# Performance work log

Hardware: AMD Instinct MI355X
Metric: run time of the kernel (lower is better)

The kernel has to match this reference:

```python
import jax, jax.numpy as jnp
import numpy as np

C = 256
NH = 4  # attention heads
G = 8   # groupnorm groups
EPS = 1e-5


def group_norm(x, weight, bias):
    B, Cc, H, W = x.shape
    xg = x.reshape(B, G, Cc // G, H, W)
    mean = xg.mean(axis=(2, 3, 4), keepdims=True)
    var = xg.var(axis=(2, 3, 4), keepdims=True)
    xg = (xg - mean) * jax.lax.rsqrt(var + EPS)
    xn = xg.reshape(B, Cc, H, W)
    return xn * weight[None, :, None, None] + bias[None, :, None, None]


def setup_inputs() -> dict:
    key = jax.random.key(0)
    ks = jax.random.split(key, 7)
    B, H, W = 16, 32, 32
    x = jax.random.normal(ks[0], (B, C, H, W), dtype=jnp.float32)
    n_weight = jnp.ones((C,), dtype=jnp.float32)
    n_bias = jnp.zeros((C,), dtype=jnp.float32)
    qkv_w = jax.random.normal(ks[1], (3 * C, C), dtype=jnp.float32) * (C ** -0.5)
    qkv_b = jnp.zeros((3 * C,), dtype=jnp.float32)
    p_w = jax.random.normal(ks[2], (C, C), dtype=jnp.float32) * (C ** -0.5)
    p_b = jnp.zeros((C,), dtype=jnp.float32)
    return {"x": x, "n_weight": n_weight, "n_bias": n_bias,
            "qkv_w": qkv_w, "qkv_b": qkv_b, "p_w": p_w, "p_b": p_b}


def reference(x, n_weight, n_bias, qkv_w, qkv_b, p_w, p_b):
    B, Cc, H, W = x.shape
    N = H * W
    dh = Cc // NH
    sc = dh ** -0.5
    xn = group_norm(x, n_weight, n_bias)  # [B,C,H,W]
    xn_flat = xn.reshape(B, Cc, N)
    # 1x1 conv == channel matmul
    qkv = jnp.einsum('oc,bcn->bon', qkv_w, xn_flat) + qkv_b[None, :, None]
    qkv = qkv.reshape(B, 3, NH, dh, N)
    q, k, v = qkv[:, 0], qkv[:, 1], qkv[:, 2]  # [B,h,dh,N]
    a = jax.nn.softmax(jnp.einsum('bhci,bhcj->bhij', q, k) * sc, axis=-1)
    o = jnp.einsum('bhij,bhcj->bhci', a, v).reshape(B, Cc, N)
    proj = jnp.einsum('oc,bcn->bon', p_w, o) + p_b[None, :, None]
    return x + proj.reshape(B, Cc, H, W)
```

## Files before the change

kernel.cpp:

```cpp
#include <hip/hip_runtime.h>
#include <math.h>

typedef unsigned short ushort;
typedef unsigned int uint;
typedef __attribute__((ext_vector_type(8))) short bf16x8;
typedef __attribute__((ext_vector_type(4))) float f32x4;

constexpr int Bc  = 16;
constexpr float EPSc = 1e-5f;

__device__ inline ushort f2bf(float f) {
    uint u = __float_as_uint(f);
    uint r = (u + 0x7fffu + ((u >> 16) & 1u)) >> 16;
    return (ushort)r;
}
__device__ inline uint pack2(float a, float b) {
    return (uint)f2bf(a) | ((uint)f2bf(b) << 16);
}
__device__ __forceinline__ void gl_lds16(const ushort* g, ushort* l) {
    __builtin_amdgcn_global_load_lds(
        (const __attribute__((address_space(1))) void*)g,
        (__attribute__((address_space(3))) void*)l, 16, 0, 0);
}

__global__ __launch_bounds__(256) void pre_k(
    const float* __restrict__ x, const float* __restrict__ qkvw,
    const float* __restrict__ pw, float* __restrict__ pstats,
    ushort* __restrict__ wqb, ushort* __restrict__ pwb) {
    int blk = blockIdx.x;
    if (blk < 512) {
        int bg = blk >> 2, part = blk & 3;
        const float4* p = (const float4*)(x + (size_t)bg * 32768 + part * 8192);
        float s = 0.f, s2 = 0.f;
        for (int i = threadIdx.x; i < 2048; i += 256) {
            float4 v = p[i];
            s += v.x + v.y + v.z + v.w;
            s2 += v.x*v.x + v.y*v.y + v.z*v.z + v.w*v.w;
        }
        __shared__ float rs[256], rq[256];
        rs[threadIdx.x] = s; rq[threadIdx.x] = s2;
        __syncthreads();
        for (int off = 128; off > 0; off >>= 1) {
            if (threadIdx.x < (unsigned)off) {
                rs[threadIdx.x] += rs[threadIdx.x + off];
                rq[threadIdx.x] += rq[threadIdx.x + off];
            }
            __syncthreads();
        }
        if (threadIdx.x == 0) {
            pstats[blk * 2]     = rs[0];
            pstats[blk * 2 + 1] = rq[0];
        }
    } else {
        int idx = ((blk - 512) * 256 + threadIdx.x) * 4;
        if (idx < 196608) {
            int row = idx >> 8;
            float sc = (row < 256) ? 0.125f : 1.f;
            float4 v = *(const float4*)&qkvw[idx];
            uint2 u; u.x = pack2(v.x * sc, v.y * sc); u.y = pack2(v.z * sc, v.w * sc);
            *(uint2*)&wqb[idx] = u;
        } else {
            int j = idx - 196608;
            float4 v = *(const float4*)&pw[j];
            uint2 u; u.x = pack2(v.x, v.y); u.y = pack2(v.z, v.w);
            *(uint2*)&pwb[j] = u;
        }
    }
}

__global__ __launch_bounds__(256) void norm_t_k(
    const float* __restrict__ x, const float* __restrict__ pstats,
    const float* __restrict__ nw, const float* __restrict__ nb,
    ushort* __restrict__ xt) {
    int b = blockIdx.z, ct = blockIdx.y, nt = blockIdx.x;
    __shared__ ushort T[64 * 72];
    int t = threadIdx.x;
    int nn4 = (t & 15) * 4;
#pragma unroll
    for (int p = 0; p < 4; ++p) {
        int cl = (t >> 4) + p * 16;
        int c = ct * 64 + cl;
        int g = c >> 5;
        int base = (b * 8 + g) * 8;
        float s  = (pstats[base] + pstats[base+2]) + (pstats[base+4] + pstats[base+6]);
        float s2 = (pstats[base+1] + pstats[base+3]) + (pstats[base+5] + pstats[base+7]);
        float inv_n = 1.f / 32768.f;
        float mean = s * inv_n;
        float var  = s2 * inv_n - mean * mean;
        float inv  = rsqrtf(var + EPSc);
        float sw = inv * nw[c];
        float sb = nb[c] - mean * sw;
        float4 v = *(const float4*)&x[((size_t)(b * 256 + c)) * 1024 + nt * 64 + nn4];
        T[(nn4 + 0) * 72 + cl] = f2bf(v.x * sw + sb);
        T[(nn4 + 1) * 72 + cl] = f2bf(v.y * sw + sb);
        T[(nn4 + 2) * 72 + cl] = f2bf(v.z * sw + sb);
        T[(nn4 + 3) * 72 + cl] = f2bf(v.w * sw + sb);
    }
    __syncthreads();
#pragma unroll
    for (int p = 0; p < 4; ++p) {
        int nn = (t >> 4) + p * 16;
        int c4 = (t & 15) * 4;
        uint2 w = *(const uint2*)&T[nn * 72 + c4];
        *(uint2*)&xt[((size_t)b * 1024 + nt * 64 + nn) * 256 + ct * 64 + c4] = w;
    }
}

__global__ __launch_bounds__(256, 2) void qkv_gemm_k(
    const ushort* __restrict__ wq, const ushort* __restrict__ xt,
    const float* __restrict__ wb, ushort* __restrict__ qkT,
    ushort* __restrict__ vbuf) {
    int b = blockIdx.z, cy = blockIdx.y, sx = blockIdx.x;
    __shared__ ushort SB[2][2][128 * 64];
    int t = threadIdx.x, lane = t & 63, w = t >> 6;
    int quad = lane >> 4, l15 = lane & 15;
    int wm = w >> 1, wn = w & 1;
    const ushort* wrow = wq + (size_t)cy * 128 * 256;
    const ushort* xrow = xt + ((size_t)b * 1024 + sx * 128) * 256;
    bool tpath = (cy < 4);
    int r0 = t >> 3;
    int cs = (t & 7) ^ (r0 & 7);
    int dst = t * 8;
#pragma unroll
    for (int ps = 0; ps < 4; ++ps) {
        int r = r0 + ps * 32;
        gl_lds16(&wrow[(size_t)r * 256 + cs * 8], &SB[0][0][ps * 2048 + dst]);
        gl_lds16(&xrow[(size_t)r * 256 + cs * 8], &SB[0][1][ps * 2048 + dst]);
    }
    __syncthreads();
    int s0 = quad ^ (l15 & 7);
    f32x4 acc[4][4] = {};
    int cur = 0;
    for (int ki = 0; ki < 4; ++ki) {
        if (ki < 3) {
            int k0 = (ki + 1) * 64, nx = cur ^ 1;
#pragma unroll
            for (int ps = 0; ps < 4; ++ps) {
                int r = r0 + ps * 32;
                gl_lds16(&wrow[(size_t)r * 256 + k0 + cs * 8], &SB[nx][0][ps * 2048 + dst]);
                gl_lds16(&xrow[(size_t)r * 256 + k0 + cs * 8], &SB[nx][1][ps * 2048 + dst]);
            }
        }
        const ushort* Wc = SB[cur][0];
        const ushort* Xc = SB[cur][1];
        const ushort* Am = tpath ? Xc : Wc;
        const ushort* Bn = tpath ? Wc : Xc;
#pragma unroll
        for (int kk = 0; kk < 2; ++kk) {
            int sl = s0 ^ (kk * 4);
            bf16x8 fa[4], fb[4];
#pragma unroll
            for (int mi = 0; mi < 4; ++mi)
                fa[mi] = *(const bf16x8*)&Am[(wm * 64 + mi * 16 + l15) * 64 + sl * 8];
#pragma unroll
            for (int ni = 0; ni < 4; ++ni)
                fb[ni] = *(const bf16x8*)&Bn[(wn * 64 + ni * 16 + l15) * 64 + sl * 8];
#pragma unroll
            for (int mi = 0; mi < 4; ++mi)
#pragma unroll
                for (int ni = 0; ni < 4; ++ni)
                    acc[mi][ni] = __builtin_amdgcn_mfma_f32_16x16x32_bf16(
                        fa[mi], fb[ni], acc[mi][ni], 0, 0, 0);
        }
        __syncthreads();
        cur ^= 1;
    }
    ushort* Tw = ((ushort*)SB) + w * (64 * 72);
    float bsc = (tpath && cy < 2) ? 0.125f : 1.f;
    if (tpath) {
#pragma unroll
        for (int ni = 0; ni < 4; ++ni) {
            float bias = wb[cy * 128 + wn * 64 + ni * 16 + l15] * bsc;
#pragma unroll
            for (int mi = 0; mi < 4; ++mi)
#pragma unroll
                for (int rr = 0; rr < 4; ++rr)
                    Tw[(mi * 16 + quad * 4 + rr) * 72 + ni * 16 + l15] =
                        f2bf(acc[mi][ni][rr] + bias);
        }
    } else {
#pragma unroll
        for (int mi = 0; mi < 4; ++mi)
#pragma unroll
            for (int rr = 0; rr < 4; ++rr) {
                float bias = wb[cy * 128 + wm * 64 + mi * 16 + quad * 4 + rr];
#pragma unroll
                for (int ni = 0; ni < 4; ++ni)
                    Tw[(mi * 16 + quad * 4 + rr) * 72 + ni * 16 + l15] =
                        f2bf(acc[mi][ni][rr] + bias);
            }
    }
    __asm__ __volatile__("" ::: "memory");
    int row8 = lane >> 3, ch = lane & 7;
#pragma unroll
    for (int p = 0; p < 8; ++p) {
        int row = p * 8 + row8;
        uint4 u = *(const uint4*)&Tw[row * 72 + ch * 8];
        if (tpath) {
            int sp = sx * 128 + wm * 64 + row;
            *(uint4*)&qkT[((size_t)b * 1024 + sp) * 512 + cy * 128 + wn * 64 + ch * 8] = u;
        } else {
            int chanloc = (cy - 4) * 128 + wm * 64 + row;
            *(uint4*)&vbuf[((size_t)b * 256 + chanloc) * 1024 + sx * 128 + wn * 64 + ch * 8] = u;
        }
    }
}

__global__ __launch_bounds__(256, 3) void attn_k(
    const ushort* __restrict__ qkT, const ushort* __restrict__ vbuf,
    ushort* __restrict__ ot) {
    int i0 = blockIdx.x * 64;
    int bh = blockIdx.y;
    int b = bh >> 2, h = bh & 3;
    const ushort* qTb = qkT + (size_t)b * 1024 * 512 + h * 64;
    const ushort* kTb = qTb + 256;
    const ushort* vb  = vbuf + ((size_t)(b * 256 + h * 64)) * 1024;
    __shared__ ushort Ks[2][4096], Vs[2][4096];
    __shared__ ushort Ps[4 * 16 * 72];
    __shared__ float  Lx[4 * 16];
    int t = threadIdx.x, lane = t & 63, w = t >> 6;
    int quad = lane >> 4, l15 = lane & 15;
    bf16x8 aq0 = *(const bf16x8*)&qTb[(size_t)(i0 + w * 16 + l15) * 512 + quad * 8];
    bf16x8 aq1 = *(const bf16x8*)&qTb[(size_t)(i0 + w * 16 + l15) * 512 + 32 + quad * 8];
    int r0 = t >> 3;
    int cs = (t & 7) ^ (r0 & 7);
    int p0 = quad ^ (l15 & 7);
    int p1 = p0 ^ 4;
    gl_lds16(&kTb[(size_t)r0 * 512 + cs * 8],        &Ks[0][t * 8]);
    gl_lds16(&kTb[(size_t)(r0 + 32) * 512 + cs * 8], &Ks[0][t * 8 + 2048]);
    gl_lds16(&vb[(size_t)r0 * 1024 + cs * 8],        &Vs[0][t * 8]);
    gl_lds16(&vb[(size_t)(r0 + 32) * 1024 + cs * 8], &Vs[0][t * 8 + 2048]);
    __syncthreads();
    float lsum = 0.f;
    f32x4 oacc[4] = {};
    int cur = 0;
    for (int j0 = 0; j0 < 1024; j0 += 64) {
        if (j0 < 960) {
            int jn = j0 + 64, nx = cur ^ 1;
            gl_lds16(&kTb[(size_t)(jn + r0) * 512 + cs * 8],        &Ks[nx][t * 8]);
            gl_lds16(&kTb[(size_t)(jn + r0 + 32) * 512 + cs * 8],   &Ks[nx][t * 8 + 2048]);
            gl_lds16(&vb[(size_t)r0 * 1024 + jn + cs * 8],          &Vs[nx][t * 8]);
            gl_lds16(&vb[(size_t)(r0 + 32) * 1024 + jn + cs * 8],   &Vs[nx][t * 8 + 2048]);
        }
        const ushort* Kc = Ks[cur];
        const ushort* Vc = Vs[cur];
        f32x4 sacc[4];
#pragma unroll
        for (int jt = 0; jt < 4; ++jt) {
            int row = jt * 16 + l15;
            f32x4 a = {0.f, 0.f, 0.f, 0.f};
            bf16x8 bk0 = *(const bf16x8*)&Kc[row * 64 + p0 * 8];
            bf16x8 bk1 = *(const bf16x8*)&Kc[row * 64 + p1 * 8];
            a = __builtin_amdgcn_mfma_f32_16x16x32_bf16(bk0, aq0, a, 0, 0, 0);
            a = __builtin_amdgcn_mfma_f32_16x16x32_bf16(bk1, aq1, a, 0, 0, 0);
            sacc[jt] = a;
        }
#pragma unroll
        for (int jt = 0; jt < 4; ++jt) {
            float e0 = __expf(sacc[jt][0]), e1 = __expf(sacc[jt][1]);
            float e2 = __expf(sacc[jt][2]), e3 = __expf(sacc[jt][3]);
            lsum += (e0 + e1) + (e2 + e3);
            int o = w * 1152 + l15 * 72 + jt * 16 + quad * 4;
            *(uint*)&Ps[o]     = pack2(e0, e1);
            *(uint*)&Ps[o + 2] = pack2(e2, e3);
        }
        __asm__ __volatile__("" ::: "memory");
        bf16x8 ap0 = *(const bf16x8*)&Ps[w * 1152 + l15 * 72 + quad * 8];
        bf16x8 ap1 = *(const bf16x8*)&Ps[w * 1152 + l15 * 72 + 32 + quad * 8];
#pragma unroll
        for (int ct = 0; ct < 4; ++ct) {
            int row = ct * 16 + l15;
            bf16x8 bv0 = *(const bf16x8*)&Vc[row * 64 + p0 * 8];
            bf16x8 bv1 = *(const bf16x8*)&Vc[row * 64 + p1 * 8];
            oacc[ct] = __builtin_amdgcn_mfma_f32_16x16x32_bf16(ap0, bv0, oacc[ct], 0, 0, 0);
            oacc[ct] = __builtin_amdgcn_mfma_f32_16x16x32_bf16(ap1, bv1, oacc[ct], 0, 0, 0);
        }
        __syncthreads();
        cur ^= 1;
    }
    lsum += __shfl_xor(lsum, 16);
    lsum += __shfl_xor(lsum, 32);
    if (quad == 0) Lx[w * 16 + l15] = lsum;
    __asm__ __volatile__("" ::: "memory");
    float4 lv = *(const float4*)&Lx[w * 16 + quad * 4];
    float linv[4] = {1.f / lv.x, 1.f / lv.y, 1.f / lv.z, 1.f / lv.w};
    ushort* Pw = &Ps[w * 1152];
#pragma unroll
    for (int ct = 0; ct < 4; ++ct)
#pragma unroll
        for (int rr = 0; rr < 4; ++rr)
            Pw[(quad * 4 + rr) * 72 + ct * 16 + l15] = f2bf(oacc[ct][rr] * linv[rr]);
    __asm__ __volatile__("" ::: "memory");
#pragma unroll
    for (int p = 0; p < 2; ++p) {
        int row = p * 8 + (lane >> 3), ch = lane & 7;
        uint4 u = *(const uint4*)&Pw[row * 72 + ch * 8];
        *(uint4*)&ot[((size_t)b * 1024 + i0 + w * 16 + row) * 256 + h * 64 + ch * 8] = u;
    }
}

__global__ __launch_bounds__(256, 2) void proj_k(
    const ushort* __restrict__ pwb, const ushort* __restrict__ ot,
    const float* __restrict__ pb, const float* __restrict__ x,
    float* __restrict__ out) {
    int b = blockIdx.z, cy = blockIdx.y, sx = blockIdx.x;
    __shared__ ushort SB[2][2][128 * 64];
    int t = threadIdx.x, lane = t & 63, w = t >> 6;
    int quad = lane >> 4, l15 = lane & 15;
    int wm = w >> 1, wn = w & 1;
    const ushort* wrow = pwb + (size_t)cy * 128 * 256;
    const ushort* xrow = ot + ((size_t)b * 1024 + sx * 128) * 256;
    int r0 = t >> 3;
    int cs = (t & 7) ^ (r0 & 7);
    int dst = t * 8;
#pragma unroll
    for (int ps = 0; ps < 4; ++ps) {
        int r = r0 + ps * 32;
        gl_lds16(&wrow[(size_t)r * 256 + cs * 8], &SB[0][0][ps * 2048 + dst]);
        gl_lds16(&xrow[(size_t)r * 256 + cs * 8], &SB[0][1][ps * 2048 + dst]);
    }
    __syncthreads();
    int s0 = quad ^ (l15 & 7);
    f32x4 acc[4][4] = {};
    int cur = 0;
    for (int ki = 0; ki < 4; ++ki) {
        if (ki < 3) {
            int k0 = (ki + 1) * 64, nx = cur ^ 1;
#pragma unroll
            for (int ps = 0; ps < 4; ++ps) {
                int r = r0 + ps * 32;
                gl_lds16(&wrow[(size_t)r * 256 + k0 + cs * 8], &SB[nx][0][ps * 2048 + dst]);
                gl_lds16(&xrow[(size_t)r * 256 + k0 + cs * 8], &SB[nx][1][ps * 2048 + dst]);
            }
        }
        const ushort* Wc = SB[cur][0];
        const ushort* Xc = SB[cur][1];
#pragma unroll
        for (int kk = 0; kk < 2; ++kk) {
            int sl = s0 ^ (kk * 4);
            bf16x8 fa[4], fb[4];
#pragma unroll
            for (int mi = 0; mi < 4; ++mi)
                fa[mi] = *(const bf16x8*)&Wc[(wm * 64 + mi * 16 + l15) * 64 + sl * 8];
#pragma unroll
            for (int ni = 0; ni < 4; ++ni)
                fb[ni] = *(const bf16x8*)&Xc[(wn * 64 + ni * 16 + l15) * 64 + sl * 8];
#pragma unroll
            for (int mi = 0; mi < 4; ++mi)
#pragma unroll
                for (int ni = 0; ni < 4; ++ni)
                    acc[mi][ni] = __builtin_amdgcn_mfma_f32_16x16x32_bf16(
                        fa[mi], fb[ni], acc[mi][ni], 0, 0, 0);
        }
        __syncthreads();
        cur ^= 1;
    }
#pragma unroll
    for (int mi = 0; mi < 4; ++mi)
#pragma unroll
        for (int rr = 0; rr < 4; ++rr) {
            int chan = cy * 128 + wm * 64 + mi * 16 + quad * 4 + rr;
            float bias = pb[chan];
#pragma unroll
            for (int ni = 0; ni < 4; ++ni) {
                int sp = sx * 128 + wn * 64 + ni * 16 + l15;
                size_t o = ((size_t)(b * 256 + chan)) * 1024 + sp;
                out[o] = acc[mi][ni][rr] + bias + x[o];
            }
        }
}

extern "C" void kernel_launch(void* const* d_in, const int* in_sizes, int n_in,
                              void* d_out, int out_size, void* d_ws, size_t ws_size,
                              hipStream_t stream) {
    const float* x    = (const float*)d_in[0];
    const float* nw   = (const float*)d_in[1];
    const float* nb   = (const float*)d_in[2];
    const float* qkvw = (const float*)d_in[3];
    const float* qkvb = (const float*)d_in[4];
    const float* pw   = (const float*)d_in[5];
    const float* pb   = (const float*)d_in[6];
    float* out = (float*)d_out;

    float* pstats = (float*)d_ws;
    ushort* base = (ushort*)((char*)d_ws + 4096);
    ushort* xt   = base;
    ushort* wqb  = xt + (size_t)16 * 1024 * 256;
    ushort* pwb  = wqb + 768 * 256;
    ushort* qkT  = pwb + 256 * 256;
    ushort* vbuf = qkT + (size_t)16 * 1024 * 512;
    ushort* ot   = xt;

    pre_k<<<dim3(768), dim3(256), 0, stream>>>(x, qkvw, pw, pstats, wqb, pwb);
    norm_t_k<<<dim3(16, 4, Bc), dim3(256), 0, stream>>>(x, pstats, nw, nb, xt);
    qkv_gemm_k<<<dim3(8, 6, Bc), dim3(256), 0, stream>>>(wqb, xt, qkvb, qkT, vbuf);
    attn_k<<<dim3(16, 64), dim3(256), 0, stream>>>(qkT, vbuf, ot);
    proj_k<<<dim3(8, 2, Bc), dim3(256), 0, stream>>>(pwb, ot, pb, x, out);
}
```

Measured before the change: 149.1 us.

## Double query rows per attention block and switch softmax to exp2 with packed bf16 conversion

The attention kernel now processes 128 query rows per block (two 16-row sub-blocks per wave), so each K/V tile staged in LDS is reused twice as often and the grid is halved. The query scale folds in log2(e), which lets the softmax use the hardware exp2 builtin, and packing uses the native cvt_pk_bf16 instruction when the compiler provides it. This trades higher register and LDS use per block, which may lower occupancy, and halves the block count to 512.

After: 138.0 us. 1.08x faster.

```diff
diff --git a/kernel.cpp b/kernel.cpp
--- a/kernel.cpp
+++ b/kernel.cpp
@@ -8,6 +8,7 @@
 
 constexpr int Bc  = 16;
 constexpr float EPSc = 1e-5f;
+constexpr float QSC  = 0.18033688f;
 
 __device__ inline ushort f2bf(float f) {
     uint u = __float_as_uint(f);
@@ -17,6 +18,19 @@
 __device__ inline uint pack2(float a, float b) {
     return (uint)f2bf(a) | ((uint)f2bf(b) << 16);
 }
+__device__ __forceinline__ uint cvt2(float a, float b) {
+#if __has_builtin(__builtin_amdgcn_cvt_pk_bf16_f32)
+    auto v = __builtin_amdgcn_cvt_pk_bf16_f32(a, b);
+    uint u; __builtin_memcpy(&u, &v, 4); return u;
+#else
+    return pack2(a, b);
+#endif
+}
+#if __has_builtin(__builtin_amdgcn_exp2f)
+#define EXP2F(x) __builtin_amdgcn_exp2f(x)
+#else
+#define EXP2F(x) __expf((x) * 0.69314718f)
+#endif
 __device__ __forceinline__ void gl_lds16(const ushort* g, ushort* l) {
     __builtin_amdgcn_global_load_lds(
         (const __attribute__((address_space(1))) void*)g,
@@ -55,7 +69,7 @@
         int idx = ((blk - 512) * 256 + threadIdx.x) * 4;
         if (idx < 196608) {
             int row = idx >> 8;
-            float sc = (row < 256) ? 0.125f : 1.f;
+            float sc = (row < 256) ? QSC : 1.f;
             float4 v = *(const float4*)&qkvw[idx];
             uint2 u; u.x = pack2(v.x * sc, v.y * sc); u.y = pack2(v.z * sc, v.w * sc);
             *(uint2*)&wqb[idx] = u;
@@ -166,7 +180,7 @@
         cur ^= 1;
     }
     ushort* Tw = ((ushort*)SB) + w * (64 * 72);
-    float bsc = (tpath && cy < 2) ? 0.125f : 1.f;
+    float bsc = (tpath && cy < 2) ? QSC : 1.f;
     if (tpath) {
 #pragma unroll
         for (int ni = 0; ni < 4; ++ni) {
@@ -209,19 +223,24 @@
 __global__ __launch_bounds__(256, 3) void attn_k(
     const ushort* __restrict__ qkT, const ushort* __restrict__ vbuf,
     ushort* __restrict__ ot) {
-    int i0 = blockIdx.x * 64;
+    int i0 = blockIdx.x * 128;
     int bh = blockIdx.y;
     int b = bh >> 2, h = bh & 3;
     const ushort* qTb = qkT + (size_t)b * 1024 * 512 + h * 64;
     const ushort* kTb = qTb + 256;
     const ushort* vb  = vbuf + ((size_t)(b * 256 + h * 64)) * 1024;
     __shared__ ushort Ks[2][4096], Vs[2][4096];
-    __shared__ ushort Ps[4 * 16 * 72];
-    __shared__ float  Lx[4 * 16];
+    __shared__ ushort Ps[8 * 1152];
+    __shared__ float  Lx[128];
     int t = threadIdx.x, lane = t & 63, w = t >> 6;
     int quad = lane >> 4, l15 = lane & 15;
-    bf16x8 aq0 = *(const bf16x8*)&qTb[(size_t)(i0 + w * 16 + l15) * 512 + quad * 8];
-    bf16x8 aq1 = *(const bf16x8*)&qTb[(size_t)(i0 + w * 16 + l15) * 512 + 32 + quad * 8];
+    bf16x8 aq[2][2];
+#pragma unroll
+    for (int rb = 0; rb < 2; ++rb) {
+        const ushort* qr = &qTb[(size_t)(i0 + rb * 64 + w * 16 + l15) * 512];
+        aq[rb][0] = *(const bf16x8*)&qr[quad * 8];
+        aq[rb][1] = *(const bf16x8*)&qr[32 + quad * 8];
+    }
     int r0 = t >> 3;
     int cs = (t & 7) ^ (r0 & 7);
     int p0 = quad ^ (l15 & 7);
@@ -231,8 +250,10 @@
     gl_lds16(&vb[(size_t)r0 * 1024 + cs * 8],        &Vs[0][t * 8]);
     gl_lds16(&vb[(size_t)(r0 + 32) * 1024 + cs * 8], &Vs[0][t * 8 + 2048]);
     __syncthreads();
-    float lsum = 0.f;
-    f32x4 oacc[4] = {};
+    float lsum0 = 0.f, lsum1 = 0.f;
+    f32x4 oacc[2][4] = {};
+    ushort* Pw0 = &Ps[(w * 2 + 0) * 1152];
+    ushort* Pw1 = &Ps[(w * 2 + 1) * 1152];
     int cur = 0;
     for (int j0 = 0; j0 < 1024; j0 += 64) {
         if (j0 < 960) {
@@ -244,58 +265,77 @@
         }
         const ushort* Kc = Ks[cur];
         const ushort* Vc = Vs[cur];
-        f32x4 sacc[4];
+        f32x4 s0[4], s1[4];
 #pragma unroll
         for (int jt = 0; jt < 4; ++jt) {
             int row = jt * 16 + l15;
-            f32x4 a = {0.f, 0.f, 0.f, 0.f};
             bf16x8 bk0 = *(const bf16x8*)&Kc[row * 64 + p0 * 8];
             bf16x8 bk1 = *(const bf16x8*)&Kc[row * 64 + p1 * 8];
-            a = __builtin_amdgcn_mfma_f32_16x16x32_bf16(bk0, aq0, a, 0, 0, 0);
-            a = __builtin_amdgcn_mfma_f32_16x16x32_bf16(bk1, aq1, a, 0, 0, 0);
-            sacc[jt] = a;
+            f32x4 a = {0.f, 0.f, 0.f, 0.f};
+            a = __builtin_amdgcn_mfma_f32_16x16x32_bf16(bk0, aq[0][0], a, 0, 0, 0);
+            a = __builtin_amdgcn_mfma_f32_16x16x32_bf16(bk1, aq[0][1], a, 0, 0, 0);
+            s0[jt] = a;
+            f32x4 c = {0.f, 0.f, 0.f, 0.f};
+            c = __builtin_amdgcn_mfma_f32_16x16x32_bf16(bk0, aq[1][0], c, 0, 0, 0);
+            c = __builtin_amdgcn_mfma_f32_16x16x32_bf16(bk1, aq[1][1], c, 0, 0, 0);
+            s1[jt] = c;
         }
 #pragma unroll
         for (int jt = 0; jt < 4; ++jt) {
-            float e0 = __expf(sacc[jt][0]), e1 = __expf(sacc[jt][1]);
-            float e2 = __expf(sacc[jt][2]), e3 = __expf(sacc[jt][3]);
-            lsum += (e0 + e1) + (e2 + e3);
-            int o = w * 1152 + l15 * 72 + jt * 16 + quad * 4;
-            *(uint*)&Ps[o]     = pack2(e0, e1);
-            *(uint*)&Ps[o + 2] = pack2(e2, e3);
+            int o = l15 * 72 + jt * 16 + quad * 4;
+            float e0 = EXP2F(s0[jt][0]), e1 = EXP2F(s0[jt][1]);
+            float e2 = EXP2F(s0[jt][2]), e3 = EXP2F(s0[jt][3]);
+            lsum0 += (e0 + e1) + (e2 + e3);
+            *(uint*)&Pw0[o]     = cvt2(e0, e1);
+            *(uint*)&Pw0[o + 2] = cvt2(e2, e3);
+            float f0 = EXP2F(s1[jt][0]), f1 = EXP2F(s1[jt][1]);
+            float f2 = EXP2F(s1[jt][2]), f3 = EXP2F(s1[jt][3]);
+            lsum1 += (f0 + f1) + (f2 + f3);
+            *(uint*)&Pw1[o]     = cvt2(f0, f1);
+            *(uint*)&Pw1[o + 2] = cvt2(f2, f3);
         }
         __asm__ __volatile__("" ::: "memory");
-        bf16x8 ap0 = *(const bf16x8*)&Ps[w * 1152 + l15 * 72 + quad * 8];
-        bf16x8 ap1 = *(const bf16x8*)&Ps[w * 1152 + l15 * 72 + 32 + quad * 8];
+        bf16x8 ap00 = *(const bf16x8*)&Pw0[l15 * 72 + quad * 8];
+        bf16x8 ap01 = *(const bf16x8*)&Pw0[l15 * 72 + 32 + quad * 8];
+        bf16x8 ap10 = *(const bf16x8*)&Pw1[l15 * 72 + quad * 8];
+        bf16x8 ap11 = *(const bf16x8*)&Pw1[l15 * 72 + 32 + quad * 8];
 #pragma unroll
         for (int ct = 0; ct < 4; ++ct) {
             int row = ct * 16 + l15;
             bf16x8 bv0 = *(const bf16x8*)&Vc[row * 64 + p0 * 8];
             bf16x8 bv1 = *(const bf16x8*)&Vc[row * 64 + p1 * 8];
-            oacc[ct] = __builtin_amdgcn_mfma_f32_16x16x32_bf16(ap0, bv0, oacc[ct], 0, 0, 0);
-            oacc[ct] = __builtin_amdgcn_mfma_f32_16x16x32_bf16(ap1, bv1, oacc[ct], 0, 0, 0);
+            oacc[0][ct] = __builtin_amdgcn_mfma_f32_16x16x32_bf16(ap00, bv0, oacc[0][ct], 0, 0, 0);
+            oacc[0][ct] = __builtin_amdgcn_mfma_f32_16x16x32_bf16(ap01, bv1, oacc[0][ct], 0, 0, 0);
+            oacc[1][ct] = __builtin_amdgcn_mfma_f32_16x16x32_bf16(ap10, bv0, oacc[1][ct], 0, 0, 0);
+            oacc[1][ct] = __builtin_amdgcn_mfma_f32_16x16x32_bf16(ap11, bv1, oacc[1][ct], 0, 0, 0);
         }
         __syncthreads();
         cur ^= 1;
     }
-    lsum += __shfl_xor(lsum, 16);
-    lsum += __shfl_xor(lsum, 32);
-    if (quad == 0) Lx[w * 16 + l15] = lsum;
+    lsum0 += __shfl_xor(lsum0, 16); lsum0 += __shfl_xor(lsum0, 32);
+    lsum1 += __shfl_xor(lsum1, 16); lsum1 += __shfl_xor(lsum1, 32);
+    if (quad == 0) {
+        Lx[w * 16 + l15]      = lsum0;
+        Lx[64 + w * 16 + l15] = lsum1;
+    }
     __asm__ __volatile__("" ::: "memory");
-    float4 lv = *(const float4*)&Lx[w * 16 + quad * 4];
-    float linv[4] = {1.f / lv.x, 1.f / lv.y, 1.f / lv.z, 1.f / lv.w};
-    ushort* Pw = &Ps[w * 1152];
-#pragma unroll
-    for (int ct = 0; ct < 4; ++ct)
-#pragma unroll
-        for (int rr = 0; rr < 4; ++rr)
-            Pw[(quad * 4 + rr) * 72 + ct * 16 + l15] = f2bf(oacc[ct][rr] * linv[rr]);
-    __asm__ __volatile__("" ::: "memory");
-#pragma unroll
-    for (int p = 0; p < 2; ++p) {
-        int row = p * 8 + (lane >> 3), ch = lane & 7;
-        uint4 u = *(const uint4*)&Pw[row * 72 + ch * 8];
-        *(uint4*)&ot[((size_t)b * 1024 + i0 + w * 16 + row) * 256 + h * 64 + ch * 8] = u;
+#pragma unroll
+    for (int rb = 0; rb < 2; ++rb) {
+        float4 lv = *(const float4*)&Lx[rb * 64 + w * 16 + quad * 4];
+        float linv[4] = {1.f / lv.x, 1.f / lv.y, 1.f / lv.z, 1.f / lv.w};
+        ushort* Pw = (rb == 0) ? Pw0 : Pw1;
+#pragma unroll
+        for (int ct = 0; ct < 4; ++ct)
+#pragma unroll
+            for (int rr = 0; rr < 4; ++rr)
+                Pw[(quad * 4 + rr) * 72 + ct * 16 + l15] = f2bf(oacc[rb][ct][rr] * linv[rr]);
+        __asm__ __volatile__("" ::: "memory");
+#pragma unroll
+        for (int p = 0; p < 2; ++p) {
+            int row = p * 8 + (lane >> 3), ch = lane & 7;
+            uint4 u = *(const uint4*)&Pw[row * 72 + ch * 8];
+            *(uint4*)&ot[((size_t)b * 1024 + i0 + rb * 64 + w * 16 + row) * 256 + h * 64 + ch * 8] = u;
+        }
     }
 }
 
@@ -394,6 +434,6 @@
     pre_k<<<dim3(768), dim3(256), 0, stream>>>(x, qkvw, pw, pstats, wqb, pwb);
     norm_t_k<<<dim3(16, 4, Bc), dim3(256), 0, stream>>>(x, pstats, nw, nb, xt);
     qkv_gemm_k<<<dim3(8, 6, Bc), dim3(256), 0, stream>>>(wqb, xt, qkvb, qkT, vbuf);
-    attn_k<<<dim3(16, 64), dim3(256), 0, stream>>>(qkT, vbuf, ot);
+    attn_k<<<dim3(8, 64), dim3(256), 0, stream>>>(qkT, vbuf, ot);
     proj_k<<<dim3(8, 2, Bc), dim3(256), 0, stream>>>(pwb, ot, pb, x, out);
 }
```
